# Kernel optimization log

Measured on AMD Instinct MI355X. Metric: run time of the kernel, lower is better.

## Reference

```python
import jax, jax.numpy as jnp
import numpy as np

NUM_BOND_TYPE = 6
NUM_BOND_DIRECTION = 3
N_NODES = 20000
N_EDGES = 320000
HIDDEN = 256
OUT = 256
N_MASK = 2000


def setup_inputs() -> dict:
    key = jax.random.key(0)
    ks = jax.random.split(key, 12)
    x = jax.random.normal(ks[0], (N_NODES, HIDDEN), dtype=jnp.float32)
    edge_index = jax.random.randint(ks[1], (2, N_EDGES), 0, N_NODES, dtype=jnp.int64)
    edge_attr = jax.random.randint(ks[2], (N_EDGES, 2), 0, 3, dtype=jnp.int64)
    mask_node_indices = jax.random.randint(ks[3], (N_MASK,), 0, N_NODES, dtype=jnp.int64)
    # parameters (torch Linear convention: y = x @ W.T + b)
    def xavier(k, shape):
        fan_in, fan_out = shape[1], shape[0]
        lim = float(np.sqrt(6.0 / (fan_in + fan_out)))
        return jax.random.uniform(k, shape, jnp.float32, -lim, lim)
    prelu_a = jnp.asarray(0.25, dtype=jnp.float32)  # torch PReLU default
    W_enc = xavier(ks[4], (HIDDEN, HIDDEN))          # enc_to_dec, no bias
    E1 = xavier(ks[5], (NUM_BOND_TYPE, HIDDEN))
    E2 = xavier(ks[6], (NUM_BOND_DIRECTION, HIDDEN))
    W1 = xavier(ks[7], (2 * HIDDEN, HIDDEN))
    b1 = jnp.zeros((2 * HIDDEN,), jnp.float32)
    W2 = xavier(ks[8], (OUT, 2 * HIDDEN))
    b2 = jnp.zeros((OUT,), jnp.float32)
    return {"x": x, "edge_index": edge_index, "edge_attr": edge_attr,
            "mask_node_indices": mask_node_indices, "prelu_a": prelu_a,
            "W_enc": W_enc, "E1": E1, "E2": E2,
            "W1": W1, "b1": b1, "W2": W2, "b2": b2}


def reference(x, edge_index, edge_attr, mask_node_indices, prelu_a,
              W_enc, E1, E2, W1, b1, W2, b2):
    N = x.shape[0]
    # PReLU -> enc_to_dec linear (no bias) -> zero masked rows
    x = jnp.where(x >= 0, x, prelu_a * x)
    x = x @ W_enc.T
    x = x.at[mask_node_indices].set(0.0)
    # add self loops: (i,i) edges with attr (4, 0)
    loop = jnp.arange(N, dtype=edge_index.dtype)
    ei = jnp.concatenate([edge_index, jnp.stack([loop, loop])], axis=1)  # [2, E+N]
    loop_attr = jnp.concatenate(
        [jnp.full((N, 1), 4, edge_attr.dtype), jnp.zeros((N, 1), edge_attr.dtype)], axis=1)
    ea = jnp.concatenate([edge_attr, loop_attr], axis=0)                 # [E+N, 2]
    edge_emb = E1[ea[:, 0]] + E2[ea[:, 1]]                               # [E+N, D]
    src, dst = ei[0], ei[1]                                              # j -> i
    msg = x[src] + edge_emb                                              # [E+N, D]
    aggr = jax.ops.segment_sum(msg, dst, num_segments=N)                 # [N, D]
    # GIN MLP: Linear -> ReLU -> Linear
    h = jax.nn.relu(aggr @ W1.T + b1)
    return h @ W2.T + b2
```

## Files before the change

### kernel.cpp

```cpp
#include <hip/hip_runtime.h>

#define HIDDEN 256
#define CAP 64

typedef _Float16 h4_t __attribute__((ext_vector_type(4)));
typedef _Float16 h8_t __attribute__((ext_vector_type(8)));
typedef float    f4_t __attribute__((ext_vector_type(4)));

typedef const __attribute__((address_space(1))) void* gbl_ptr_t;
typedef __attribute__((address_space(3))) void*       lds_ptr_t;

__device__ inline f4_t cvt4(h4_t h) {
    f4_t o; o.x = (float)h.x; o.y = (float)h.y; o.z = (float)h.z; o.w = (float)h.w;
    return o;
}

__global__ __launch_bounds__(256) void k_init(
        int* __restrict__ cnt, unsigned char* __restrict__ flags,
        const int* __restrict__ mask, int N, int Mpad, int NM) {
    int b = blockIdx.x, t = threadIdx.x;
    if (b == 0) {
        unsigned int* f4p = (unsigned int*)flags;
        for (int i = t; i < Mpad / 4; i += 256) f4p[i] = 0;
        __syncthreads();
        for (int i = t; i < NM; i += 256) flags[mask[i]] = 1;
        return;
    }
    int i = (b - 1) * 256 + t;
    if (i < N) cnt[i] = 0;
}

__global__ __launch_bounds__(128) void k_gemm1_prep(
        const float* __restrict__ x, const float* __restrict__ W_enc,
        const float* __restrict__ prelu_a, _Float16* __restrict__ XEh,
        const unsigned char* __restrict__ flags,
        const int* __restrict__ ei, const int* __restrict__ ea, int E,
        int* __restrict__ cnt, int* __restrict__ csr,
        const float* __restrict__ W1, const float* __restrict__ W2,
        _Float16* __restrict__ Wh1, _Float16* __restrict__ Wh2,
        int N, int NT, int nb_fill) {
    __shared__ __align__(16) _Float16 As[64 * 32];
    __shared__ __align__(16) _Float16 Bs[128 * 32];
    int b = blockIdx.x, t = threadIdx.x;

    if (b >= NT) {
        int u = b - NT;
        if (u < nb_fill) {
            int e = u * 128 + t;
            if (e < E) {
                int src = ei[e];
                int dst = ei[E + e];
                int combo = ea[2 * e] * 3 + ea[2 * e + 1];
                int slot = atomicAdd(&cnt[dst], 1);
                if (slot < CAP) csr[dst * CAP + slot] = src | (combo << 16);
            }
        } else {
            const int n1 = 2 * HIDDEN * HIDDEN;
            int base = ((u - nb_fill) * 128 + t) * 4;
            const float* s; _Float16* d; int off;
            if (base < n1) { s = W1; d = Wh1; off = base; }
            else           { s = W2; d = Wh2; off = base - n1; }
            f4_t v = *(const f4_t*)(s + off);
            h4_t o; o.x = (_Float16)v.x; o.y = (_Float16)v.y;
            o.z = (_Float16)v.z; o.w = (_Float16)v.w;
            *(h4_t*)(d + off) = o;
        }
        return;
    }

    int w = t >> 6, L = t & 63;
    int wc = w * 64;
    int m0 = (b >> 1) * 64, n0 = (b & 1) * 128;
    int lr = L & 15, lk = (L >> 4) * 8;
    float pa = *prelu_a;

    f4_t acc[4][4] = {};
    f4_t fa32[2][2];
    f4_t fb32[4][2];

    auto LOADG = [&](int k0) {
#pragma unroll
        for (int i = 0; i < 2; ++i) {
            int c = t + 128 * i;
            int row = m0 + (c >> 2), col = k0 + (c & 3) * 8;
            if (row < N) {
                const float* p = x + (size_t)row * HIDDEN + col;
                fa32[i][0] = *(const f4_t*)p;
                fa32[i][1] = *(const f4_t*)(p + 4);
            } else {
                fa32[i][0] = (f4_t){0.f, 0.f, 0.f, 0.f};
                fa32[i][1] = (f4_t){0.f, 0.f, 0.f, 0.f};
            }
        }
#pragma unroll
        for (int i = 0; i < 4; ++i) {
            int c = t + 128 * i;
            const float* p = W_enc + (size_t)(n0 + (c >> 2)) * HIDDEN + k0 + (c & 3) * 8;
            fb32[i][0] = *(const f4_t*)p;
            fb32[i][1] = *(const f4_t*)(p + 4);
        }
    };
    auto CVTW = [&]() {
#pragma unroll
        for (int i = 0; i < 2; ++i) {
            int c = t + 128 * i;
            f4_t u = fa32[i][0], v = fa32[i][1];
            h8_t o;
            o[0] = (_Float16)(u.x >= 0.f ? u.x : pa * u.x);
            o[1] = (_Float16)(u.y >= 0.f ? u.y : pa * u.y);
            o[2] = (_Float16)(u.z >= 0.f ? u.z : pa * u.z);
            o[3] = (_Float16)(u.w >= 0.f ? u.w : pa * u.w);
            o[4] = (_Float16)(v.x >= 0.f ? v.x : pa * v.x);
            o[5] = (_Float16)(v.y >= 0.f ? v.y : pa * v.y);
            o[6] = (_Float16)(v.z >= 0.f ? v.z : pa * v.z);
            o[7] = (_Float16)(v.w >= 0.f ? v.w : pa * v.w);
            *(h8_t*)&As[c * 8] = o;
        }
#pragma unroll
        for (int i = 0; i < 4; ++i) {
            int c = t + 128 * i;
            f4_t u = fb32[i][0], v = fb32[i][1];
            h8_t o;
            o[0] = (_Float16)u.x; o[1] = (_Float16)u.y;
            o[2] = (_Float16)u.z; o[3] = (_Float16)u.w;
            o[4] = (_Float16)v.x; o[5] = (_Float16)v.y;
            o[6] = (_Float16)v.z; o[7] = (_Float16)v.w;
            *(h8_t*)&Bs[c * 8] = o;
        }
    };

    LOADG(0);
    constexpr int NS = HIDDEN / 32;
#pragma unroll
    for (int s = 0; s < NS; ++s) {
        CVTW();
        asm volatile("s_waitcnt lgkmcnt(0)" ::: "memory");
        __syncthreads();
        h8_t af[4], bf[4];
#pragma unroll
        for (int i = 0; i < 4; ++i) af[i] = *(const h8_t*)&As[(i * 16 + lr) * 32 + lk];
#pragma unroll
        for (int j = 0; j < 4; ++j) bf[j] = *(const h8_t*)&Bs[(wc + j * 16 + lr) * 32 + lk];
        asm volatile("s_waitcnt lgkmcnt(0)" ::: "memory");
        __syncthreads();
        if (s + 1 < NS) LOADG((s + 1) * 32);
#pragma unroll
        for (int i = 0; i < 4; ++i)
#pragma unroll
            for (int j = 0; j < 4; ++j)
                acc[i][j] = __builtin_amdgcn_mfma_f32_16x16x32_f16(af[i], bf[j], acc[i][j], 0, 0, 0);
    }

    int lr4 = (L >> 4) * 4;
#pragma unroll
    for (int i = 0; i < 4; ++i)
#pragma unroll
        for (int r = 0; r < 4; ++r) {
            int row = m0 + i * 16 + lr4 + r;
            float zm = flags[row] ? 0.f : 1.f;
#pragma unroll
            for (int j = 0; j < 4; ++j) {
                int col = n0 + wc + j * 16 + lr;
                XEh[(size_t)row * HIDDEN + col] = (_Float16)(acc[i][j][r] * zm);
            }
        }
}

__global__ __launch_bounds__(256) void k_aggregate(
        const _Float16* __restrict__ xe,
        const float* __restrict__ E1, const float* __restrict__ E2,
        const int* __restrict__ cnt, const int* __restrict__ csr,
        _Float16* __restrict__ aggr, int N, int Mpad) {
    __shared__ __align__(16) _Float16 e12h[18 * HIDDEN];
    int t = threadIdx.x;
    for (int idx = t; idx < 18 * 64; idx += 256) {
        int combo = idx >> 6, c4 = (idx & 63) * 4;
        int a1 = combo / 3, a2 = combo - a1 * 3;
        f4_t v1 = *(const f4_t*)(E1 + a1 * HIDDEN + c4);
        f4_t v2 = *(const f4_t*)(E2 + a2 * HIDDEN + c4);
        h4_t o;
        o.x = (_Float16)(v1.x + v2.x); o.y = (_Float16)(v1.y + v2.y);
        o.z = (_Float16)(v1.z + v2.z); o.w = (_Float16)(v1.w + v2.w);
        *(h4_t*)(e12h + combo * HIDDEN + c4) = o;
    }
    __syncthreads();
    int node = blockIdx.x * 4 + (t >> 6);
    if (node >= Mpad) return;
    int lane = t & 63;
    int c0 = lane * 4;
    if (node >= N) {
        *(h4_t*)(aggr + (size_t)node * HIDDEN + c0) = (h4_t)(_Float16)0.f;
        return;
    }
    int deg = cnt[node];
    if (deg > CAP) deg = CAP;
    const int* lst = csr + (size_t)node * CAP;
    int pv = (lane < deg) ? lst[lane] : 0;

    h4_t hs = *(const h4_t*)(xe + (size_t)node * HIDDEN + c0);
    h4_t se = *(const h4_t*)(e12h + 12 * HIDDEN + c0);
    f4_t acc = cvt4(hs) + cvt4(se);

    int e = 0;
    for (; e + 7 < deg; e += 8) {
        int p[8]; h4_t hv[8], qv[8];
#pragma unroll
        for (int j = 0; j < 8; ++j) p[j] = __shfl(pv, e + j, 64);
#pragma unroll
        for (int j = 0; j < 8; ++j)
            hv[j] = *(const h4_t*)(xe + (size_t)(p[j] & 0xFFFF) * HIDDEN + c0);
#pragma unroll
        for (int j = 0; j < 8; ++j)
            qv[j] = *(const h4_t*)(e12h + (p[j] >> 16) * HIDDEN + c0);
        h4_t s0 = (hv[0] + qv[0]) + (hv[1] + qv[1]);
        h4_t s1 = (hv[2] + qv[2]) + (hv[3] + qv[3]);
        h4_t s2 = (hv[4] + qv[4]) + (hv[5] + qv[5]);
        h4_t s3 = (hv[6] + qv[6]) + (hv[7] + qv[7]);
        acc += cvt4(s0) + cvt4(s1);
        acc += cvt4(s2) + cvt4(s3);
    }
    for (; e < deg; ++e) {
        int p = __shfl(pv, e, 64);
        h4_t h = *(const h4_t*)(xe + (size_t)(p & 0xFFFF) * HIDDEN + c0);
        h4_t q = *(const h4_t*)(e12h + (p >> 16) * HIDDEN + c0);
        acc += cvt4(h + q);
    }
    h4_t o;
    o.x = (_Float16)acc.x; o.y = (_Float16)acc.y;
    o.z = (_Float16)acc.z; o.w = (_Float16)acc.w;
    *(h4_t*)(aggr + (size_t)node * HIDDEN + c0) = o;
}

template <int K, bool RELU, bool HAS_BIAS, bool OUT_F16, bool MASK>
__global__ __launch_bounds__(128) void k_gemm64x128(
        const _Float16* __restrict__ A, const _Float16* __restrict__ B,
        const float* __restrict__ bias, void* __restrict__ Cout,
        const unsigned char* __restrict__ flags, int Mstore, int N) {
    __shared__ __align__(16) _Float16 As[64 * 32];
    __shared__ __align__(16) _Float16 Bs[128 * 32];
    int t = threadIdx.x;
    int w = t >> 6, L = t & 63;
    int wc = w * 64;
    int m0 = blockIdx.y * 64, n0 = blockIdx.x * 128;
    int lr = L & 15, lk = (L >> 4) * 8;

    f4_t acc[4][4] = {};

    auto stage = [&](int k0) {
#pragma unroll
        for (int i = 0; i < 2; ++i) {
            int c = t + 128 * i;
            __builtin_amdgcn_global_load_lds(
                (gbl_ptr_t)(A + (size_t)(m0 + (c >> 2)) * K + k0 + (c & 3) * 8),
                (lds_ptr_t)(As + c * 8), 16, 0, 0);
        }
#pragma unroll
        for (int i = 0; i < 4; ++i) {
            int c = t + 128 * i;
            __builtin_amdgcn_global_load_lds(
                (gbl_ptr_t)(B + (size_t)(n0 + (c >> 2)) * K + k0 + (c & 3) * 8),
                (lds_ptr_t)(Bs + c * 8), 16, 0, 0);
        }
    };

    stage(0);
    constexpr int NS = K / 32;
#pragma unroll
    for (int s = 0; s < NS; ++s) {
        asm volatile("s_waitcnt vmcnt(0)" ::: "memory");
        __syncthreads();
        h8_t af[4], bf[4];
#pragma unroll
        for (int i = 0; i < 4; ++i) af[i] = *(const h8_t*)&As[(i * 16 + lr) * 32 + lk];
#pragma unroll
        for (int j = 0; j < 4; ++j) bf[j] = *(const h8_t*)&Bs[(wc + j * 16 + lr) * 32 + lk];
        asm volatile("s_waitcnt lgkmcnt(0)" ::: "memory");
        __syncthreads();
        if (s + 1 < NS) stage((s + 1) * 32);
#pragma unroll
        for (int i = 0; i < 4; ++i)
#pragma unroll
            for (int j = 0; j < 4; ++j)
                acc[i][j] = __builtin_amdgcn_mfma_f32_16x16x32_f16(af[i], bf[j], acc[i][j], 0, 0, 0);
    }

    int lr4 = (L >> 4) * 4;
#pragma unroll
    for (int i = 0; i < 4; ++i)
#pragma unroll
        for (int r = 0; r < 4; ++r) {
            int row = m0 + i * 16 + lr4 + r;
            float zm = 1.f;
            if constexpr (MASK) zm = flags[row] ? 0.f : 1.f;
#pragma unroll
            for (int j = 0; j < 4; ++j) {
                int col = n0 + wc + j * 16 + lr;
                float v = acc[i][j][r];
                if constexpr (HAS_BIAS) v += bias[col];
                if constexpr (RELU) v = v > 0.f ? v : 0.f;
                v *= zm;
                if constexpr (OUT_F16) {
                    ((_Float16*)Cout)[(size_t)row * N + col] = (_Float16)v;
                } else {
                    if (row < Mstore) ((float*)Cout)[(size_t)row * N + col] = v;
                }
            }
        }
}

extern "C" void kernel_launch(void* const* d_in, const int* in_sizes, int n_in,
                              void* d_out, int out_size, void* d_ws, size_t ws_size,
                              hipStream_t stream) {
    const float* x       = (const float*)d_in[0];
    const int*   ei      = (const int*)d_in[1];
    const int*   ea      = (const int*)d_in[2];
    const int*   mask    = (const int*)d_in[3];
    const float* prelu_a = (const float*)d_in[4];
    const float* W_enc   = (const float*)d_in[5];
    const float* E1      = (const float*)d_in[6];
    const float* E2      = (const float*)d_in[7];
    const float* W1      = (const float*)d_in[8];
    const float* b1      = (const float*)d_in[9];
    const float* W2      = (const float*)d_in[10];
    const float* b2      = (const float*)d_in[11];
    float*       out     = (float*)d_out;

    int N  = in_sizes[0] / HIDDEN;
    int E  = in_sizes[1] / 2;
    int NM = in_sizes[3];
    int Mpad = ((N + 127) / 128) * 128;

    char* ws = (char*)d_ws;
    size_t off = 0;
    _Float16* XEh   = (_Float16*)(ws + off); off += (size_t)Mpad * HIDDEN * 2;
    _Float16* AGh   = (_Float16*)(ws + off); off += (size_t)Mpad * HIDDEN * 2;
    _Float16* Hh    = (_Float16*)(ws + off); off += (size_t)Mpad * 2 * HIDDEN * 2;
    _Float16* Wh1   = (_Float16*)(ws + off); off += (size_t)2 * HIDDEN * HIDDEN * 2;
    _Float16* Wh2   = (_Float16*)(ws + off); off += (size_t)HIDDEN * 2 * HIDDEN * 2;
    int* cnt        = (int*)(ws + off);      off += (size_t)N * 4;
    unsigned char* flags = (unsigned char*)(ws + off); off += (size_t)Mpad;
    off = (off + 15) & ~(size_t)15;
    int* csr        = (int*)(ws + off);      off += (size_t)N * CAP * 4;

    k_init<<<1 + (N + 255) / 256, 256, 0, stream>>>(cnt, flags, mask, N, Mpad, NM);

    int NT      = (Mpad / 64) * (HIDDEN / 128);
    int nb_fill = (E + 127) / 128;
    int nb_w    = (2 * 2 * HIDDEN * HIDDEN / 4) / 128;
    k_gemm1_prep<<<NT + nb_fill + nb_w, 128, 0, stream>>>(
        x, W_enc, prelu_a, XEh, flags,
        ei, ea, E, cnt, csr, W1, W2, Wh1, Wh2,
        N, NT, nb_fill);

    k_aggregate<<<(Mpad + 3) / 4, 256, 0, stream>>>(XEh, E1, E2, cnt, csr, AGh, N, Mpad);

    dim3 g2(2 * HIDDEN / 128, Mpad / 64);
    k_gemm64x128<HIDDEN, true, true, true, false><<<g2, 128, 0, stream>>>(
        AGh, Wh1, b1, Hh, nullptr, N, 2 * HIDDEN);

    dim3 g3(HIDDEN / 128, Mpad / 64);
    k_gemm64x128<2 * HIDDEN, false, true, false, false><<<g3, 128, 0, stream>>>(
        Hh, Wh2, b2, out, nullptr, N, HIDDEN);
}
```

Measured before the change: 172.0 us.

## Double-buffer GEMM LDS tiles with two-stage lookahead prefetch

```diff
diff --git a/kernel.cpp b/kernel.cpp
--- a/kernel.cpp
+++ b/kernel.cpp
@@ -9,6 +9,16 @@
 
 typedef const __attribute__((address_space(1))) void* gbl_ptr_t;
 typedef __attribute__((address_space(3))) void*       lds_ptr_t;
+
+template<int N> struct IC { static constexpr int v = N; };
+template<int...> struct Seq {};
+template<int N, int... Is> struct MkSeq : MkSeq<N - 1, N - 1, Is...> {};
+template<int... Is> struct MkSeq<0, Is...> { using t = Seq<Is...>; };
+template<typename F, int... Is>
+__device__ __forceinline__ void unroll_for(F&& f, Seq<Is...>) { (f(IC<Is>{}), ...); }
+template<int N> __device__ __forceinline__ void vmwait() {
+    asm volatile("s_waitcnt vmcnt(%0)" :: "n"(N) : "memory");
+}
 
 __device__ inline f4_t cvt4(h4_t h) {
     f4_t o; o.x = (float)h.x; o.y = (float)h.y; o.z = (float)h.z; o.w = (float)h.w;
@@ -236,8 +246,8 @@
         const _Float16* __restrict__ A, const _Float16* __restrict__ B,
         const float* __restrict__ bias, void* __restrict__ Cout,
         const unsigned char* __restrict__ flags, int Mstore, int N) {
-    __shared__ __align__(16) _Float16 As[64 * 32];
-    __shared__ __align__(16) _Float16 Bs[128 * 32];
+    __shared__ __align__(16) _Float16 As[2][64 * 32];
+    __shared__ __align__(16) _Float16 Bs[2][128 * 32];
     int t = threadIdx.x;
     int w = t >> 6, L = t & 63;
     int wc = w * 64;
@@ -246,43 +256,48 @@
 
     f4_t acc[4][4] = {};
 
-    auto stage = [&](int k0) {
+    auto stage = [&](int s) {
+        int k0 = s * 32, r = s & 1;
 #pragma unroll
         for (int i = 0; i < 2; ++i) {
             int c = t + 128 * i;
             __builtin_amdgcn_global_load_lds(
                 (gbl_ptr_t)(A + (size_t)(m0 + (c >> 2)) * K + k0 + (c & 3) * 8),
-                (lds_ptr_t)(As + c * 8), 16, 0, 0);
+                (lds_ptr_t)(As[r] + c * 8), 16, 0, 0);
         }
 #pragma unroll
         for (int i = 0; i < 4; ++i) {
             int c = t + 128 * i;
             __builtin_amdgcn_global_load_lds(
                 (gbl_ptr_t)(B + (size_t)(n0 + (c >> 2)) * K + k0 + (c & 3) * 8),
-                (lds_ptr_t)(Bs + c * 8), 16, 0, 0);
+                (lds_ptr_t)(Bs[r] + c * 8), 16, 0, 0);
         }
     };
 
+    constexpr int NS = K / 32;
     stage(0);
-    constexpr int NS = K / 32;
-#pragma unroll
-    for (int s = 0; s < NS; ++s) {
-        asm volatile("s_waitcnt vmcnt(0)" ::: "memory");
+    if constexpr (NS > 1) stage(1);
+
+    unroll_for([&](auto SC) {
+        constexpr int s = SC.v;
+        vmwait<(s + 1 < NS) ? 6 : 0>();
         __syncthreads();
         h8_t af[4], bf[4];
-#pragma unroll
-        for (int i = 0; i < 4; ++i) af[i] = *(const h8_t*)&As[(i * 16 + lr) * 32 + lk];
-#pragma unroll
-        for (int j = 0; j < 4; ++j) bf[j] = *(const h8_t*)&Bs[(wc + j * 16 + lr) * 32 + lk];
+        const _Float16* as = As[s & 1];
+        const _Float16* bs = Bs[s & 1];
+#pragma unroll
+        for (int i = 0; i < 4; ++i) af[i] = *(const h8_t*)&as[(i * 16 + lr) * 32 + lk];
+#pragma unroll
+        for (int j = 0; j < 4; ++j) bf[j] = *(const h8_t*)&bs[(wc + j * 16 + lr) * 32 + lk];
         asm volatile("s_waitcnt lgkmcnt(0)" ::: "memory");
         __syncthreads();
-        if (s + 1 < NS) stage((s + 1) * 32);
+        if constexpr (s + 2 < NS) stage(s + 2);
 #pragma unroll
         for (int i = 0; i < 4; ++i)
 #pragma unroll
             for (int j = 0; j < 4; ++j)
                 acc[i][j] = __builtin_amdgcn_mfma_f32_16x16x32_f16(af[i], bf[j], acc[i][j], 0, 0, 0);
-    }
+    }, typename MkSeq<NS>::t{});
 
     int lr4 = (L >> 4) * 4;
 #pragma unroll
```

New measurement: 178.0 us. +3.5%, slower.
